# Optimization experiments

Measured on AMD Instinct MI355X. Metric: run time of the kernel, lower is better.

Reference implementation:

```python
import jax, jax.numpy as jnp
import numpy as np

B, T, D, KDIM = 256, 512, 256, 256

def setup_inputs() -> dict:
    key = jax.random.key(0)
    k1, k2, k3 = jax.random.split(key, 3)
    inputs = jax.random.normal(k1, (B, T, D), dtype=jnp.float32)
    # glorot-style scaling for stability of the recurrence
    U = jax.random.normal(k2, (D, KDIM), dtype=jnp.float32) * (1.0 / np.sqrt(D))
    W = jax.random.normal(k3, (KDIM, KDIM), dtype=jnp.float32) * (1.0 / np.sqrt(KDIM))
    b = jnp.zeros((KDIM,), dtype=jnp.float32)
    return {"inputs": inputs, "U": U, "W": W, "b": b}

def reference(inputs, U, W, b):
    # vanilla RNN: h_t = tanh(x_t U + h_{t-1} W + b); returns final hidden state
    xU = jnp.einsum('btd,dk->btk', inputs, U) + b  # precompute input projection [B,T,K]

    def step(h, xu_t):
        h = jnp.tanh(xu_t + h @ W)
        return h, None

    h0 = jnp.zeros((inputs.shape[0], W.shape[0]), dtype=inputs.dtype)
    h_final, _ = jax.lax.scan(step, h0, jnp.swapaxes(xU, 0, 1))  # scan over time
    # original keras code keeps a singleton time axis on the state: [B,1,K]
    return h_final[:, None, :]
```

## Files before the change

kernel.cpp:

```cpp
#include <hip/hip_runtime.h>
#include <hip/hip_bf16.h>


typedef _Float16 half8_t __attribute__((ext_vector_type(8)));
typedef _Float16 half2_t __attribute__((ext_vector_type(2)));
typedef float    float4_t __attribute__((ext_vector_type(4)));

#define MFMA16(a, b, c) __builtin_amdgcn_mfma_f32_16x16x32_f16((a), (b), (c), 0, 0, 0)

__device__ __forceinline__ half2_t pk_h2(float a, float b) {
    auto r = __builtin_amdgcn_cvt_pkrtz(a, b);
    return __builtin_bit_cast(half2_t, r);
}

__device__ __forceinline__ float fast_tanh(float x) {
    float e = __expf(2.0f * x);
    return 1.0f - 2.0f * __builtin_amdgcn_rcpf(e + 1.0f);
}

__global__ void transpose_u(const float* __restrict__ U, _Float16* __restrict__ Ut) {
    int id = blockIdx.x * 256 + threadIdx.x;
    int d = id >> 8, n = id & 255;
    Ut[n * 264 + d] = (_Float16)U[id];
}

__global__ __launch_bounds__(256, 2) void xu_gemm(
    const float* __restrict__ x,
    const _Float16* __restrict__ Ut,
    half2_t* __restrict__ xu)
{
    __shared__ char lds[61440];
    const int tid = threadIdx.x;
    const int lane = tid & 63, w = tid >> 6, l15 = lane & 15, q = lane >> 4;
    const int bx = blockIdx.x;
    const int t_blk = bx >> 1;
    const int b0 = (bx & 1) * 128;

    float4 ar[4];
    uint4  br[4];

    auto loadA = [&](int it) {
#pragma unroll
        for (int i = 0; i < 4; ++i) {
            int u = tid + 256 * i, row = u >> 3, seg = u & 7;
            ar[i] = *(const float4*)(x + ((size_t)(b0 + row) * 512 + t_blk) * 256
                                       + it * 32 + seg * 4);
        }
    };
    auto loadB = [&](int it) {
#pragma unroll
        for (int i = 0; i < 4; ++i) {
            int u = tid + 256 * i, p = u >> 2, seg = u & 3;
            int c = 32 * (p >> 5) + 2 * (p & 15) + ((p >> 4) & 1);
            br[i] = *(const uint4*)((const char*)Ut + c * 528 + it * 64 + seg * 16);
        }
    };
    auto writeAB = [&](int s) {
        char* As = lds + s * 10240;
        char* Bs = lds + 20480 + s * 20480;
#pragma unroll
        for (int i = 0; i < 4; ++i) {
            int u = tid + 256 * i, row = u >> 3, seg = u & 7;
            half2_t p0 = pk_h2(ar[i].x, ar[i].y);
            half2_t p1 = pk_h2(ar[i].z, ar[i].w);
            uint2 v;
            v.x = __builtin_bit_cast(unsigned, p0);
            v.y = __builtin_bit_cast(unsigned, p1);
            *(uint2*)(As + row * 80 + seg * 8) = v;
        }
#pragma unroll
        for (int i = 0; i < 4; ++i) {
            int u = tid + 256 * i, p = u >> 2, seg = u & 3;
            *(uint4*)(Bs + p * 80 + seg * 16) = br[i];
        }
    };

    float4_t acc[32];
#pragma unroll
    for (int i = 0; i < 32; ++i) { acc[i][0] = 0.f; acc[i][1] = 0.f; acc[i][2] = 0.f; acc[i][3] = 0.f; }

    loadA(0); loadB(0); writeAB(0);
    __syncthreads();

    for (int it = 0; it < 8; ++it) {
        if (it < 7) { loadA(it + 1); loadB(it + 1); }
        const char* As = lds + (it & 1) * 10240;
        const char* Bs = lds + 20480 + (it & 1) * 20480;
        half8_t af[2];
#pragma unroll
        for (int ms = 0; ms < 2; ++ms)
            af[ms] = *(const half8_t*)(As + (32 * w + 16 * ms + l15) * 80 + q * 16);
#pragma unroll
        for (int ns = 0; ns < 16; ++ns) {
            half8_t bf = *(const half8_t*)(Bs + (16 * ns + l15) * 80 + q * 16);
            acc[ns * 2 + 0] = MFMA16(af[0], bf, acc[ns * 2 + 0]);
            acc[ns * 2 + 1] = MFMA16(af[1], bf, acc[ns * 2 + 1]);
        }
        if (it < 7) writeAB((it + 1) & 1);
        __syncthreads();
    }

#pragma unroll
    for (int ms = 0; ms < 2; ++ms)
#pragma unroll
        for (int j = 0; j < 8; ++j)
#pragma unroll
            for (int i = 0; i < 4; ++i) {
                float v0 = acc[(2 * j) * 2 + ms][i];
                float v1 = acc[(2 * j + 1) * 2 + ms][i];
                half2_t p = pk_h2(v0, v1);
                int m_g = bx * 128 + 32 * w + 16 * ms + q * 4 + i;
                int c = 32 * j + 2 * l15;
                xu[(size_t)m_g * 128 + (c >> 1)] = p;
            }
}

__global__ __launch_bounds__(512, 2) void rnn_scan(
    const half2_t* __restrict__ xu,
    const float* __restrict__ W,
    const float* __restrict__ bias,
    float* __restrict__ out)
{
    __shared__ char lds[16896];
    const int tid = threadIdx.x;
    const int lane = tid & 63, w = tid >> 6, l15 = lane & 15, q = lane >> 4;
    const int blk = blockIdx.x;
    const int c0 = 32 * w + 2 * l15;

    half8_t wf[2][8];
#pragma unroll
    for (int tt = 0; tt < 2; ++tt)
#pragma unroll
        for (int c = 0; c < 8; ++c) {
            half8_t f;
#pragma unroll
            for (int j = 0; j < 8; ++j) {
                int k = 32 * c + q * 8 + j;
                f[j] = (_Float16)W[k * 256 + c0 + tt];
            }
            wf[tt][c] = f;
        }
    const float b0 = bias[c0], b1 = bias[c0 + 1];

    for (int i = tid; i < 16896 / 4; i += 512) ((int*)lds)[i] = 0;

    const int rowg0 = 16 * blk + q * 4;
    half2_t xu_n[4];
    {
        int xb = (0 * 256 + rowg0) * 128 + (c0 >> 1);
#pragma unroll
        for (int i = 0; i < 4; ++i) xu_n[i] = xu[xb + i * 128];
    }
    __syncthreads();

    char* const hbuf0 = (char*)lds;
    char* const hbuf1 = (char*)lds + 8448;

    for (int t = 0; t < 512; ++t) {
        float4_t acc0, acc1;
#pragma unroll
        for (int i = 0; i < 4; ++i) { acc0[i] = (float)xu_n[i][0]; acc1[i] = (float)xu_n[i][1]; }

        int tn = (t < 511) ? (t + 1) : 511;
        int xb = (tn * 256 + rowg0) * 128 + (c0 >> 1);
#pragma unroll
        for (int i = 0; i < 4; ++i) xu_n[i] = xu[xb + i * 128];

        const char* hcur = (t & 1) ? hbuf1 : hbuf0;
        half8_t af[8];
#pragma unroll
        for (int c = 0; c < 8; ++c)
            af[c] = *(const half8_t*)(hcur + l15 * 528 + c * 64 + q * 16);

#pragma unroll
        for (int c = 0; c < 8; ++c) {
            acc0 = MFMA16(af[c], wf[0][c], acc0);
            acc1 = MFMA16(af[c], wf[1][c], acc1);
        }

        if (t == 511) {
#pragma unroll
            for (int i = 0; i < 4; ++i) {
                float v0 = fast_tanh(acc0[i] + b0);
                float v1 = fast_tanh(acc1[i] + b1);
                float2 st; st.x = v0; st.y = v1;
                *(float2*)(&out[(rowg0 + i) * 256 + c0]) = st;
            }
        } else {
            char* hnext = ((t + 1) & 1) ? hbuf1 : hbuf0;
#pragma unroll
            for (int i = 0; i < 4; ++i) {
                float v0 = fast_tanh(acc0[i] + b0);
                float v1 = fast_tanh(acc1[i] + b1);
                half2_t p = pk_h2(v0, v1);
                *(half2_t*)(hnext + (q * 4 + i) * 528 + c0 * 2) = p;
            }
        }
        __syncthreads();
    }
}

extern "C" void kernel_launch(void* const* d_in, const int* in_sizes, int n_in,
                              void* d_out, int out_size, void* d_ws, size_t ws_size,
                              hipStream_t stream) {
    const float* x = (const float*)d_in[0];
    const float* U = (const float*)d_in[1];
    const float* W = (const float*)d_in[2];
    const float* b = (const float*)d_in[3];
    float* out = (float*)d_out;

    char* ws = (char*)d_ws;
    _Float16* Ut = (_Float16*)ws;
    half2_t*  xu = (half2_t*)(ws + 262144);

    transpose_u<<<256, 256, 0, stream>>>(U, Ut);
    xu_gemm<<<1024, 256, 0, stream>>>(x, Ut, xu);
    rnn_scan<<<16, 512, 0, stream>>>(xu, W, b, out);
}
```

Before: 542.6 us.

## Store xU batch-major, fold bias into GEMM, prefetch xU four steps ahead in scan

The input-projection GEMM now processes rows in natural [B,T] order, so its x reads are contiguous, and it adds the bias in the epilogue. The recurrent scan no longer handles bias. It keeps a 4-deep register ring of xU values so each global load has several timesteps to arrive before use. The MFMA chain is split into two independent accumulators to shorten the dependency chain, and tanh uses exp2 directly. This costs more registers in the latency-bound scan, and the per-row xU reads become strided by T.

```diff
diff --git a/kernel.cpp b/kernel.cpp
--- a/kernel.cpp
+++ b/kernel.cpp
@@ -14,7 +14,7 @@
 }
 
 __device__ __forceinline__ float fast_tanh(float x) {
-    float e = __expf(2.0f * x);
+    float e = __builtin_amdgcn_exp2f(2.8853900817779268f * x);
     return 1.0f - 2.0f * __builtin_amdgcn_rcpf(e + 1.0f);
 }
 
@@ -27,14 +27,14 @@
 __global__ __launch_bounds__(256, 2) void xu_gemm(
     const float* __restrict__ x,
     const _Float16* __restrict__ Ut,
+    const float* __restrict__ bias,
     half2_t* __restrict__ xu)
 {
     __shared__ char lds[61440];
     const int tid = threadIdx.x;
     const int lane = tid & 63, w = tid >> 6, l15 = lane & 15, q = lane >> 4;
     const int bx = blockIdx.x;
-    const int t_blk = bx >> 1;
-    const int b0 = (bx & 1) * 128;
+    const size_t m0 = (size_t)bx * 128;
 
     float4 ar[4];
     uint4  br[4];
@@ -43,8 +43,7 @@
 #pragma unroll
         for (int i = 0; i < 4; ++i) {
             int u = tid + 256 * i, row = u >> 3, seg = u & 7;
-            ar[i] = *(const float4*)(x + ((size_t)(b0 + row) * 512 + t_blk) * 256
-                                       + it * 32 + seg * 4);
+            ar[i] = *(const float4*)(x + (m0 + row) * 256 + it * 32 + seg * 4);
         }
     };
     auto loadB = [&](int it) {
@@ -103,22 +102,23 @@
 #pragma unroll
     for (int ms = 0; ms < 2; ++ms)
 #pragma unroll
-        for (int j = 0; j < 8; ++j)
+        for (int j = 0; j < 8; ++j) {
+            const int c = 32 * j + 2 * l15;
+            const float2 bb = *(const float2*)(bias + c);
 #pragma unroll
             for (int i = 0; i < 4; ++i) {
-                float v0 = acc[(2 * j) * 2 + ms][i];
-                float v1 = acc[(2 * j + 1) * 2 + ms][i];
+                float v0 = acc[(2 * j) * 2 + ms][i] + bb.x;
+                float v1 = acc[(2 * j + 1) * 2 + ms][i] + bb.y;
                 half2_t p = pk_h2(v0, v1);
                 int m_g = bx * 128 + 32 * w + 16 * ms + q * 4 + i;
-                int c = 32 * j + 2 * l15;
                 xu[(size_t)m_g * 128 + (c >> 1)] = p;
             }
+        }
 }
 
 __global__ __launch_bounds__(512, 2) void rnn_scan(
     const half2_t* __restrict__ xu,
     const float* __restrict__ W,
-    const float* __restrict__ bias,
     float* __restrict__ out)
 {
     __shared__ char lds[16896];
@@ -140,63 +140,75 @@
             }
             wf[tt][c] = f;
         }
-    const float b0 = bias[c0], b1 = bias[c0 + 1];
 
     for (int i = tid; i < 16896 / 4; i += 512) ((int*)lds)[i] = 0;
 
     const int rowg0 = 16 * blk + q * 4;
-    half2_t xu_n[4];
-    {
-        int xb = (0 * 256 + rowg0) * 128 + (c0 >> 1);
-#pragma unroll
-        for (int i = 0; i < 4; ++i) xu_n[i] = xu[xb + i * 128];
-    }
+    const int colh = c0 >> 1;
+
+    half2_t xr[4][4];
+#pragma unroll
+    for (int p = 0; p < 4; ++p)
+#pragma unroll
+        for (int i = 0; i < 4; ++i)
+            xr[p][i] = xu[((rowg0 + i) * 512 + p) * 128 + colh];
+
     __syncthreads();
 
     char* const hbuf0 = (char*)lds;
     char* const hbuf1 = (char*)lds + 8448;
 
-    for (int t = 0; t < 512; ++t) {
-        float4_t acc0, acc1;
-#pragma unroll
-        for (int i = 0; i < 4; ++i) { acc0[i] = (float)xu_n[i][0]; acc1[i] = (float)xu_n[i][1]; }
-
-        int tn = (t < 511) ? (t + 1) : 511;
-        int xb = (tn * 256 + rowg0) * 128 + (c0 >> 1);
-#pragma unroll
-        for (int i = 0; i < 4; ++i) xu_n[i] = xu[xb + i * 128];
-
-        const char* hcur = (t & 1) ? hbuf1 : hbuf0;
-        half8_t af[8];
-#pragma unroll
-        for (int c = 0; c < 8; ++c)
-            af[c] = *(const half8_t*)(hcur + l15 * 528 + c * 64 + q * 16);
-
-#pragma unroll
-        for (int c = 0; c < 8; ++c) {
-            acc0 = MFMA16(af[c], wf[0][c], acc0);
-            acc1 = MFMA16(af[c], wf[1][c], acc1);
-        }
-
-        if (t == 511) {
+    for (int t4 = 0; t4 < 512; t4 += 4) {
+#pragma unroll
+        for (int p = 0; p < 4; ++p) {
+            const int t = t4 + p;
+
+            float4_t a0a, a1a, a0b, a1b;
 #pragma unroll
             for (int i = 0; i < 4; ++i) {
-                float v0 = fast_tanh(acc0[i] + b0);
-                float v1 = fast_tanh(acc1[i] + b1);
-                float2 st; st.x = v0; st.y = v1;
-                *(float2*)(&out[(rowg0 + i) * 256 + c0]) = st;
-            }
-        } else {
-            char* hnext = ((t + 1) & 1) ? hbuf1 : hbuf0;
-#pragma unroll
-            for (int i = 0; i < 4; ++i) {
-                float v0 = fast_tanh(acc0[i] + b0);
-                float v1 = fast_tanh(acc1[i] + b1);
-                half2_t p = pk_h2(v0, v1);
-                *(half2_t*)(hnext + (q * 4 + i) * 528 + c0 * 2) = p;
-            }
-        }
-        __syncthreads();
+                a0a[i] = (float)xr[p][i][0];
+                a1a[i] = (float)xr[p][i][1];
+                a0b[i] = 0.f; a1b[i] = 0.f;
+            }
+
+            const char* hcur = (t & 1) ? hbuf1 : hbuf0;
+            half8_t af[8];
+#pragma unroll
+            for (int c = 0; c < 8; ++c)
+                af[c] = *(const half8_t*)(hcur + l15 * 528 + c * 64 + q * 16);
+
+            const int tn = (t + 4 <= 511) ? (t + 4) : 511;
+#pragma unroll
+            for (int i = 0; i < 4; ++i)
+                xr[p][i] = xu[((rowg0 + i) * 512 + tn) * 128 + colh];
+
+#pragma unroll
+            for (int c = 0; c < 4; ++c) {
+                a0a = MFMA16(af[2 * c],     wf[0][2 * c],     a0a);
+                a1a = MFMA16(af[2 * c],     wf[1][2 * c],     a1a);
+                a0b = MFMA16(af[2 * c + 1], wf[0][2 * c + 1], a0b);
+                a1b = MFMA16(af[2 * c + 1], wf[1][2 * c + 1], a1b);
+            }
+
+            if (t == 511) {
+#pragma unroll
+                for (int i = 0; i < 4; ++i) {
+                    float v0 = fast_tanh(a0a[i] + a0b[i]);
+                    float v1 = fast_tanh(a1a[i] + a1b[i]);
+                    float2 st; st.x = v0; st.y = v1;
+                    *(float2*)(&out[(rowg0 + i) * 256 + c0]) = st;
+                }
+            } else {
+                char* hnext = ((t + 1) & 1) ? hbuf1 : hbuf0;
+#pragma unroll
+                for (int i = 0; i < 4; ++i) {
+                    float v0 = fast_tanh(a0a[i] + a0b[i]);
+                    float v1 = fast_tanh(a1a[i] + a1b[i]);
+                    *(half2_t*)(hnext + (q * 4 + i) * 528 + c0 * 2) = pk_h2(v0, v1);
+                }
+            }
+            __syncthreads();
+        }
     }
 }
 
@@ -214,6 +226,6 @@
     half2_t*  xu = (half2_t*)(ws + 262144);
 
     transpose_u<<<256, 256, 0, stream>>>(U, Ut);
-    xu_gemm<<<1024, 256, 0, stream>>>(x, Ut, xu);
-    rnn_scan<<<16, 512, 0, stream>>>(xu, W, b, out);
-}
+    xu_gemm<<<1024, 256, 0, stream>>>(x, Ut, b, xu);
+    rnn_scan<<<16, 512, 0, stream>>>(xu, W, out);
+}
```

New measurement: 525.8 us. -3.1%, faster.
